# Optimization experiments

Hardware: AMD Instinct MI355X
Metric: run time of the kernel (lower is better)

Reference implementation:

```python
import jax, jax.numpy as jnp
import numpy as np

B, D, K, A = 32768, 256, 1024, 32
MIN_LOG_STD, MAX_LOG_STD = -20.0, 2.0


def setup_inputs() -> dict:
    key = jax.random.key(0)
    ks = jax.random.split(key, 9)
    return {
        "obs": jax.random.normal(ks[0], (B, D), dtype=jnp.float32),
        "mean_C": jax.random.normal(ks[1], (K, D), dtype=jnp.float32),
        "mean_sigma": jnp.abs(jax.random.normal(ks[2], (K,), dtype=jnp.float32)) + 0.1,
        "mean_w": jax.random.normal(ks[3], (A, K), dtype=jnp.float32),
        "mean_b": jax.random.normal(ks[4], (A,), dtype=jnp.float32),
        "std_C": jax.random.normal(ks[5], (K, D), dtype=jnp.float32),
        "std_sigma": jnp.abs(jax.random.normal(ks[6], (K,), dtype=jnp.float32)) + 0.1,
        "std_w": jax.random.normal(ks[7], (A, K), dtype=jnp.float32),
        "std_b": jax.random.normal(ks[8], (A,), dtype=jnp.float32),
    }


def _rbf(x, C, sigma_sq, w, b):
    # r[b,k] = sum_d (x[b,d] - C[k,d])^2, expanded to avoid a [B,K,D] intermediate
    x2 = jnp.sum(x * x, axis=-1, keepdims=True)           # [B,1]
    c2 = jnp.sum(C * C, axis=-1)[None, :]                  # [1,K]
    r = x2 - 2.0 * (x @ C.T) + c2                          # [B,K]
    phi = jnp.exp(-r / (2.0 * jnp.abs(sigma_sq)[None, :]))  # [B,K]
    return phi @ w.T + b[None, :]                          # [B,A]


def reference(obs, mean_C, mean_sigma, mean_w, mean_b,
              std_C, std_sigma, std_w, std_b):
    action_mean = _rbf(obs, mean_C, mean_sigma, mean_w, mean_b)
    std_raw = _rbf(obs, std_C, std_sigma, std_w, std_b)
    action_std = jnp.exp(jnp.clip(std_raw, MIN_LOG_STD, MAX_LOG_STD))
    return jnp.concatenate((action_mean, action_std), axis=-1)  # [B, 2A]
```

## Files before the change

kernel.cpp:

```cpp
#include <hip/hip_runtime.h>


typedef float floatx4 __attribute__((ext_vector_type(4)));
typedef long longx2 __attribute__((ext_vector_type(2)));
typedef unsigned int u32;
typedef unsigned char u8;

constexpr float LOG2E = 1.4426950408889634f;

__device__ __forceinline__ u32 pk_fp8(float a, float b, float c, float d) {
  u32 v = __builtin_amdgcn_cvt_pk_fp8_f32(a, b, 0u, 0);
  v = __builtin_amdgcn_cvt_pk_fp8_f32(c, d, v, 1);
  return v;
}
__device__ __forceinline__ long mk64(u32 lo, u32 hi) {
  return (long)lo | ((long)hi << 32);
}

__global__ void prep(const float* __restrict__ mC, const float* __restrict__ mS,
                     const float* __restrict__ sC, const float* __restrict__ sS,
                     const float* __restrict__ mw, const float* __restrict__ sw,
                     u8* __restrict__ Cb2, float* __restrict__ a2g,
                     float* __restrict__ g2n, u8* __restrict__ wb)
{
  const int blk = blockIdx.x;
  if (blk < 512) {
    const int wq = threadIdx.x >> 6;
    const int t  = threadIdx.x & 63;
    const int b  = blk * 4 + wq;
    const int half = b >> 10;
    const int k = b & 1023;
    const float* src = (half ? sC : mC) + (size_t)k * 256;
    float4 f = *(const float4*)(src + t * 4);
    float ss = f.x*f.x + f.y*f.y + f.z*f.z + f.w*f.w;
    const int ct = b >> 6, row = b & 63;
    const int wvv = row >> 4, cc = row & 15;
    const int ks = t >> 3, qq = (t >> 1) & 3, rr = (t & 1) * 4;
    *(u32*)(Cb2 + (size_t)ct * 16384 + wvv * 4096 + (qq * 16 + cc) * 64 + ks * 8 + rr) =
        pk_fp8(f.x, f.y, f.z, f.w);
    for (int off = 32; off > 0; off >>= 1) ss += __shfl_down(ss, off, 64);
    if (t == 0) {
      float sig = fabsf((half ? sS : mS)[k]);
      float s2 = LOG2E * 0.5f / sig;
      a2g[b] = 2.f * s2;
      g2n[b] = -s2 * ss;
    }
  } else {
    int i0 = (blk - 512) * 1024 + threadIdx.x * 4;
    int half = i0 >> 15;
    int rem  = i0 & 32767;
    const float* src = half ? sw : mw;
    float4 f = *(const float4*)(src + rem);
    ((u32*)wb)[i0 >> 2] = pk_fp8(f.x, f.y, f.z, f.w);
  }
}

__global__ __launch_bounds__(256, 2)
void policy_main(const float* __restrict__ obs,
                 const u8* __restrict__ Cb2,
                 const float* __restrict__ a2g,
                 const float* __restrict__ g2n,
                 const u8* __restrict__ wb,
                 const float* __restrict__ mbias,
                 const float* __restrict__ sbias,
                 float* __restrict__ out)
{
  __shared__ __align__(16) char smem[69888];
  float* x2p = (float*)(smem + 16384);
  float* red = (float*)smem;

  const int tid  = threadIdx.x;
  const int lane = tid & 63;
  const int wv   = tid >> 6;
  const int c    = lane & 15;
  const int q    = lane >> 4;
  const int row0 = blockIdx.x * 64;
  const int kslc = 16 * wv + 4 * q;
  const int cfo  = tid * 64;

  long cfPA[8], cfPB[8], cfQA[8], cfQB[8];
  #pragma unroll
  for (int i = 0; i < 4; ++i) {
    longx2 t0 = *(const longx2*)(Cb2 + cfo + i * 16);
    cfPA[2 * i] = t0.x; cfPA[2 * i + 1] = t0.y;
    longx2 t1 = *(const longx2*)(Cb2 + 16384 + cfo + i * 16);
    cfPB[2 * i] = t1.x; cfPB[2 * i + 1] = t1.y;
  }

  #pragma unroll
  for (int i = 0; i < 4; ++i) {
    int s = i * 256 + tid;
    int row = s >> 4;
    int s16 = s & 15;
    int l16 = s16 ^ (row & 15);
    const float* src = obs + (size_t)(row0 + row) * 256 + l16 * 16;
    float4 f0 = ((const float4*)src)[0];
    float4 f1 = ((const float4*)src)[1];
    float4 f2 = ((const float4*)src)[2];
    float4 f3 = ((const float4*)src)[3];
    uint4 pk;
    pk.x = pk_fp8(f0.x, f0.y, f0.z, f0.w);
    pk.y = pk_fp8(f1.x, f1.y, f1.z, f1.w);
    pk.z = pk_fp8(f2.x, f2.y, f2.z, f2.w);
    pk.w = pk_fp8(f3.x, f3.y, f3.z, f3.w);
    *(uint4*)(smem + s * 16) = pk;
    float p = f0.x*f0.x + f0.y*f0.y + f0.z*f0.z + f0.w*f0.w
            + f1.x*f1.x + f1.y*f1.y + f1.z*f1.z + f1.w*f1.w
            + f2.x*f2.x + f2.y*f2.y + f2.z*f2.z + f2.w*f2.w
            + f3.x*f3.x + f3.y*f3.y + f3.z*f3.z + f3.w*f3.w;
    x2p[row * 16 + s16] = p;
  }
  __syncthreads();

  long ob[4][8];
  #pragma unroll
  for (int nt = 0; nt < 4; ++nt) {
    const int row = nt * 16 + c;
    #pragma unroll
    for (int ks = 0; ks < 8; ++ks) {
      int cc8 = 4 * ks + q;
      int s16 = (cc8 >> 1) ^ (row & 15);
      ob[nt][ks] = *(const long*)(smem + row * 256 + s16 * 16 + (q & 1) * 8);
    }
  }
  if (tid < 64) {
    float s = 0.f;
    #pragma unroll
    for (int j = 0; j < 16; j += 4) {
      float4 a = *(const float4*)(x2p + tid * 16 + j);
      s += a.x + a.y + a.z + a.w;
    }
    x2p[1024 + tid] = s;
  }
  __syncthreads();

  float hx2[4];
  #pragma unroll
  for (int nt = 0; nt < 4; ++nt) hx2[nt] = 0.5f * x2p[1024 + nt * 16 + c];

  const floatx4 Z4 = {0.f, 0.f, 0.f, 0.f};
  floatx4 acc2m[2][4], acc2s[2][4];
  #pragma unroll
  for (int a2i = 0; a2i < 2; ++a2i)
    #pragma unroll
    for (int nt = 0; nt < 4; ++nt) {
      acc2m[a2i][nt] = Z4;
      acc2s[a2i][nt] = Z4;
    }

  u32 pE[4], pc[4];

#define PAIR_BODY(pr, CA, CB, NA, NB, ACC, HB)                                          \
  {                                                                                     \
    const int cte = 2 * (pr);                                                           \
    if ((pr) < 15) {                                                                    \
      const u8* g0 = Cb2 + (size_t)(cte + 2) * 16384 + cfo;                             \
      _Pragma("unroll")                                                                 \
      for (int i = 0; i < 4; ++i) {                                                     \
        longx2 t0 = *(const longx2*)(g0 + i * 16);                                      \
        NA[2 * i] = t0.x; NA[2 * i + 1] = t0.y;                                         \
        longx2 t1 = *(const longx2*)(g0 + 16384 + i * 16);                              \
        NB[2 * i] = t1.x; NB[2 * i + 1] = t1.y;                                         \
      }                                                                                 \
    }                                                                                   \
    float4 a2e = *(const float4*)(a2g + cte * 64 + kslc);                               \
    float4 g2e = *(const float4*)(g2n + cte * 64 + kslc);                               \
    float4 a2o = *(const float4*)(a2g + cte * 64 + 64 + kslc);                          \
    float4 g2o = *(const float4*)(g2n + cte * 64 + 64 + kslc);                          \
    const int kbE = (cte & 15) * 64 + kslc;                                             \
    const u8* wr0 = wb + (size_t)((HB) + c) * 1024 + kbE;                               \
    const u8* wr1 = wb + (size_t)((HB) + 16 + c) * 1024 + kbE;                          \
    u32 w0lo = *(const u32*)wr0, w0hi = *(const u32*)(wr0 + 64);                        \
    u32 w1lo = *(const u32*)wr1, w1hi = *(const u32*)(wr1 + 64);                        \
    floatx4 a1[4];                                                                      \
    a1[0] = __builtin_amdgcn_mfma_f32_16x16x32_fp8_fp8(CA[0], ob[0][0], Z4, 0, 0, 0);   \
    a1[1] = __builtin_amdgcn_mfma_f32_16x16x32_fp8_fp8(CA[0], ob[1][0], Z4, 0, 0, 0);   \
    a1[2] = __builtin_amdgcn_mfma_f32_16x16x32_fp8_fp8(CA[0], ob[2][0], Z4, 0, 0, 0);   \
    a1[3] = __builtin_amdgcn_mfma_f32_16x16x32_fp8_fp8(CA[0], ob[3][0], Z4, 0, 0, 0);   \
    _Pragma("unroll")                                                                   \
    for (int ks = 1; ks < 8; ++ks) {                                                    \
      a1[0] = __builtin_amdgcn_mfma_f32_16x16x32_fp8_fp8(CA[ks], ob[0][ks], a1[0], 0, 0, 0); \
      a1[1] = __builtin_amdgcn_mfma_f32_16x16x32_fp8_fp8(CA[ks], ob[1][ks], a1[1], 0, 0, 0); \
      a1[2] = __builtin_amdgcn_mfma_f32_16x16x32_fp8_fp8(CA[ks], ob[2][ks], a1[2], 0, 0, 0); \
      a1[3] = __builtin_amdgcn_mfma_f32_16x16x32_fp8_fp8(CA[ks], ob[3][ks], a1[3], 0, 0, 0); \
    }                                                                                   \
    _Pragma("unroll")                                                                   \
    for (int nt = 0; nt < 4; ++nt) {                                                    \
      float t0 = a1[nt][0] - hx2[nt], t1 = a1[nt][1] - hx2[nt];                         \
      float t2 = a1[nt][2] - hx2[nt], t3 = a1[nt][3] - hx2[nt];                         \
      pE[nt] = pk_fp8(__builtin_amdgcn_exp2f(fmaf(a2e.x, t0, g2e.x)),                   \
                      __builtin_amdgcn_exp2f(fmaf(a2e.y, t1, g2e.y)),                   \
                      __builtin_amdgcn_exp2f(fmaf(a2e.z, t2, g2e.z)),                   \
                      __builtin_amdgcn_exp2f(fmaf(a2e.w, t3, g2e.w)));                  \
    }                                                                                   \
    a1[0] = __builtin_amdgcn_mfma_f32_16x16x32_fp8_fp8(CB[0], ob[0][0], Z4, 0, 0, 0);   \
    a1[1] = __builtin_amdgcn_mfma_f32_16x16x32_fp8_fp8(CB[0], ob[1][0], Z4, 0, 0, 0);   \
    a1[2] = __builtin_amdgcn_mfma_f32_16x16x32_fp8_fp8(CB[0], ob[2][0], Z4, 0, 0, 0);   \
    a1[3] = __builtin_amdgcn_mfma_f32_16x16x32_fp8_fp8(CB[0], ob[3][0], Z4, 0, 0, 0);   \
    _Pragma("unroll")                                                                   \
    for (int ks = 1; ks < 8; ++ks) {                                                    \
      a1[0] = __builtin_amdgcn_mfma_f32_16x16x32_fp8_fp8(CB[ks], ob[0][ks], a1[0], 0, 0, 0); \
      a1[1] = __builtin_amdgcn_mfma_f32_16x16x32_fp8_fp8(CB[ks], ob[1][ks], a1[1], 0, 0, 0); \
      a1[2] = __builtin_amdgcn_mfma_f32_16x16x32_fp8_fp8(CB[ks], ob[2][ks], a1[2], 0, 0, 0); \
      a1[3] = __builtin_amdgcn_mfma_f32_16x16x32_fp8_fp8(CB[ks], ob[3][ks], a1[3], 0, 0, 0); \
    }                                                                                   \
    _Pragma("unroll")                                                                   \
    for (int nt = 0; nt < 4; ++nt) {                                                    \
      float t0 = a1[nt][0] - hx2[nt], t1 = a1[nt][1] - hx2[nt];                         \
      float t2 = a1[nt][2] - hx2[nt], t3 = a1[nt][3] - hx2[nt];                         \
      pc[nt] = pk_fp8(__builtin_amdgcn_exp2f(fmaf(a2o.x, t0, g2o.x)),                   \
                      __builtin_amdgcn_exp2f(fmaf(a2o.y, t1, g2o.y)),                   \
                      __builtin_amdgcn_exp2f(fmaf(a2o.z, t2, g2o.z)),                   \
                      __builtin_amdgcn_exp2f(fmaf(a2o.w, t3, g2o.w)));                  \
    }                                                                                   \
    { long wA0 = mk64(w0lo, w0hi), wA1 = mk64(w1lo, w1hi);                              \
      _Pragma("unroll")                                                                 \
      for (int nt = 0; nt < 4; ++nt) {                                                  \
        long pb = mk64(pE[nt], pc[nt]);                                                 \
        ACC[0][nt] = __builtin_amdgcn_mfma_f32_16x16x32_fp8_fp8(wA0, pb, ACC[0][nt], 0, 0, 0); \
        ACC[1][nt] = __builtin_amdgcn_mfma_f32_16x16x32_fp8_fp8(wA1, pb, ACC[1][nt], 0, 0, 0); \
      } }                                                                               \
  }

  for (int pr = 0; pr < 8; pr += 2) {
    PAIR_BODY(pr,     cfPA, cfPB, cfQA, cfQB, acc2m, 0)
    PAIR_BODY(pr + 1, cfQA, cfQB, cfPA, cfPB, acc2m, 0)
  }
  for (int pr = 8; pr < 16; pr += 2) {
    PAIR_BODY(pr,     cfPA, cfPB, cfQA, cfQB, acc2s, 32)
    PAIR_BODY(pr + 1, cfQA, cfQB, cfPA, cfPB, acc2s, 32)
  }
#undef PAIR_BODY

  {
    float* myr = red + wv * 4352;
    #pragma unroll
    for (int a2i = 0; a2i < 2; ++a2i)
      #pragma unroll
      for (int nt = 0; nt < 4; ++nt) {
        *(floatx4*)(myr + (nt * 16 + c) * 68 + a2i * 16 + 4 * q)      = acc2m[a2i][nt];
        *(floatx4*)(myr + (nt * 16 + c) * 68 + 32 + a2i * 16 + 4 * q) = acc2s[a2i][nt];
      }
  }
  __syncthreads();

  #pragma unroll
  for (int i = 0; i < 16; ++i) {
    int idx = tid + 256 * i;
    int a = idx & 63;
    int b = idx >> 6;
    float v = red[b * 68 + a] + red[4352 + b * 68 + a] +
              red[8704 + b * 68 + a] + red[13056 + b * 68 + a];
    if (a < 32) {
      v += mbias[a];
    } else {
      v += sbias[a - 32];
      v = fminf(fmaxf(v, -20.f), 2.f);
      v = __builtin_amdgcn_exp2f(v * LOG2E);
    }
    out[(size_t)(row0 + b) * 64 + a] = v;
  }
}

extern "C" void kernel_launch(void* const* d_in, const int* in_sizes, int n_in,
                              void* d_out, int out_size, void* d_ws, size_t ws_size,
                              hipStream_t stream) {
  const float* obs = (const float*)d_in[0];
  const float* mC  = (const float*)d_in[1];
  const float* mS  = (const float*)d_in[2];
  const float* mW  = (const float*)d_in[3];
  const float* mB  = (const float*)d_in[4];
  const float* sC  = (const float*)d_in[5];
  const float* sS  = (const float*)d_in[6];
  const float* sW  = (const float*)d_in[7];
  const float* sB  = (const float*)d_in[8];
  float* out = (float*)d_out;

  u8*    Cb2 = (u8*)d_ws;
  float* a2g = (float*)((char*)d_ws + 2048 * 256);
  float* g2n = a2g + 2048;
  u8*    wb  = (u8*)(g2n + 2048);

  prep<<<576, 256, 0, stream>>>(mC, mS, sC, sS, mW, sW, Cb2, a2g, g2n, wb);
  policy_main<<<512, 256, 0, stream>>>(obs, Cb2, a2g, g2n, wb, mB, sB, out);
}
```

Measured before the change: 130.1 us.

## Switch first distance GEMM from fp8 to int8 MFMA with fixed-scale quantization

Quantizes obs and centers to int8 with a fixed scale (clamped at about ±5) and uses 16x16x64 i8 MFMA instead of 16x16x32 fp8 for the x·C product. This halves the MFMA instruction count for the first GEMM and loads operands as 16-byte vectors. The squared norms and exponent scale factors are recomputed in the quantized domain so the RBF stays consistent. Fixed-scale int8 changes rounding behaviour and clips values beyond the range, which may affect accuracy.

```diff
diff --git a/kernel.cpp b/kernel.cpp
--- a/kernel.cpp
+++ b/kernel.cpp
@@ -2,11 +2,13 @@
 
 
 typedef float floatx4 __attribute__((ext_vector_type(4)));
-typedef long longx2 __attribute__((ext_vector_type(2)));
+typedef int   intx4  __attribute__((ext_vector_type(4)));
 typedef unsigned int u32;
 typedef unsigned char u8;
 
 constexpr float LOG2E = 1.4426950408889634f;
+constexpr float QS    = 25.4f;
+constexpr float SINV2 = (5.0f / 127.0f) * (5.0f / 127.0f);
 
 __device__ __forceinline__ u32 pk_fp8(float a, float b, float c, float d) {
   u32 v = __builtin_amdgcn_cvt_pk_fp8_f32(a, b, 0u, 0);
@@ -15,6 +17,12 @@
 }
 __device__ __forceinline__ long mk64(u32 lo, u32 hi) {
   return (long)lo | ((long)hi << 32);
+}
+__device__ __forceinline__ int q8(float x) {
+  return (int)rintf(fminf(fmaxf(x * QS, -127.f), 127.f));
+}
+__device__ __forceinline__ u32 pk_i8(int a, int b, int c, int d) {
+  return (u32)(a & 255) | ((u32)(b & 255) << 8) | ((u32)(c & 255) << 16) | ((u32)(d & 255) << 24);
 }
 
 __global__ void prep(const float* __restrict__ mC, const float* __restrict__ mS,
@@ -32,18 +40,19 @@
     const int k = b & 1023;
     const float* src = (half ? sC : mC) + (size_t)k * 256;
     float4 f = *(const float4*)(src + t * 4);
-    float ss = f.x*f.x + f.y*f.y + f.z*f.z + f.w*f.w;
+    int i0 = q8(f.x), i1 = q8(f.y), i2 = q8(f.z), i3 = q8(f.w);
     const int ct = b >> 6, row = b & 63;
     const int wvv = row >> 4, cc = row & 15;
-    const int ks = t >> 3, qq = (t >> 1) & 3, rr = (t & 1) * 4;
-    *(u32*)(Cb2 + (size_t)ct * 16384 + wvv * 4096 + (qq * 16 + cc) * 64 + ks * 8 + rr) =
-        pk_fp8(f.x, f.y, f.z, f.w);
-    for (int off = 32; off > 0; off >>= 1) ss += __shfl_down(ss, off, 64);
+    const int ks = t >> 4, qq = (t >> 2) & 3, j0 = (t & 3) * 4;
+    *(u32*)(Cb2 + (size_t)ct * 16384 + wvv * 4096 + (16 * qq + cc) * 64 + 16 * ks + j0) =
+        pk_i8(i0, i1, i2, i3);
+    int is = i0 * i0 + i1 * i1 + i2 * i2 + i3 * i3;
+    for (int off = 32; off > 0; off >>= 1) is += __shfl_down(is, off, 64);
     if (t == 0) {
       float sig = fabsf((half ? sS : mS)[k]);
-      float s2 = LOG2E * 0.5f / sig;
-      a2g[b] = 2.f * s2;
-      g2n[b] = -s2 * ss;
+      float t2 = SINV2 * LOG2E * 0.5f / sig;
+      a2g[b] = 2.f * t2;
+      g2n[b] = -t2 * (float)is;
     }
   } else {
     int i0 = (blk - 512) * 1024 + threadIdx.x * 4;
@@ -78,13 +87,11 @@
   const int kslc = 16 * wv + 4 * q;
   const int cfo  = tid * 64;
 
-  long cfPA[8], cfPB[8], cfQA[8], cfQB[8];
+  intx4 cfPA[4], cfPB[4], cfQA[4], cfQB[4];
   #pragma unroll
   for (int i = 0; i < 4; ++i) {
-    longx2 t0 = *(const longx2*)(Cb2 + cfo + i * 16);
-    cfPA[2 * i] = t0.x; cfPA[2 * i + 1] = t0.y;
-    longx2 t1 = *(const longx2*)(Cb2 + 16384 + cfo + i * 16);
-    cfPB[2 * i] = t1.x; cfPB[2 * i + 1] = t1.y;
+    cfPA[i] = *(const intx4*)(Cb2 + cfo + i * 16);
+    cfPB[i] = *(const intx4*)(Cb2 + 16384 + cfo + i * 16);
   }
 
   #pragma unroll
@@ -98,29 +105,32 @@
     float4 f1 = ((const float4*)src)[1];
     float4 f2 = ((const float4*)src)[2];
     float4 f3 = ((const float4*)src)[3];
+    int a0 = q8(f0.x), a1v = q8(f0.y), a2v = q8(f0.z), a3 = q8(f0.w);
+    int b0 = q8(f1.x), b1 = q8(f1.y), b2 = q8(f1.z), b3 = q8(f1.w);
+    int c0 = q8(f2.x), c1 = q8(f2.y), c2 = q8(f2.z), c3 = q8(f2.w);
+    int d0 = q8(f3.x), d1 = q8(f3.y), d2 = q8(f3.z), d3 = q8(f3.w);
     uint4 pk;
-    pk.x = pk_fp8(f0.x, f0.y, f0.z, f0.w);
-    pk.y = pk_fp8(f1.x, f1.y, f1.z, f1.w);
-    pk.z = pk_fp8(f2.x, f2.y, f2.z, f2.w);
-    pk.w = pk_fp8(f3.x, f3.y, f3.z, f3.w);
+    pk.x = pk_i8(a0, a1v, a2v, a3);
+    pk.y = pk_i8(b0, b1, b2, b3);
+    pk.z = pk_i8(c0, c1, c2, c3);
+    pk.w = pk_i8(d0, d1, d2, d3);
     *(uint4*)(smem + s * 16) = pk;
-    float p = f0.x*f0.x + f0.y*f0.y + f0.z*f0.z + f0.w*f0.w
-            + f1.x*f1.x + f1.y*f1.y + f1.z*f1.z + f1.w*f1.w
-            + f2.x*f2.x + f2.y*f2.y + f2.z*f2.z + f2.w*f2.w
-            + f3.x*f3.x + f3.y*f3.y + f3.z*f3.z + f3.w*f3.w;
-    x2p[row * 16 + s16] = p;
+    int is = a0*a0 + a1v*a1v + a2v*a2v + a3*a3
+           + b0*b0 + b1*b1 + b2*b2 + b3*b3
+           + c0*c0 + c1*c1 + c2*c2 + c3*c3
+           + d0*d0 + d1*d1 + d2*d2 + d3*d3;
+    x2p[row * 16 + s16] = (float)is;
   }
   __syncthreads();
 
-  long ob[4][8];
+  intx4 ob[4][4];
   #pragma unroll
   for (int nt = 0; nt < 4; ++nt) {
     const int row = nt * 16 + c;
     #pragma unroll
-    for (int ks = 0; ks < 8; ++ks) {
-      int cc8 = 4 * ks + q;
-      int s16 = (cc8 >> 1) ^ (row & 15);
-      ob[nt][ks] = *(const long*)(smem + row * 256 + s16 * 16 + (q & 1) * 8);
+    for (int ks = 0; ks < 4; ++ks) {
+      int slot = (4 * ks + q) ^ (row & 15);
+      ob[nt][ks] = *(const intx4*)(smem + row * 256 + slot * 16);
     }
   }
   if (tid < 64) {
@@ -138,6 +148,7 @@
   #pragma unroll
   for (int nt = 0; nt < 4; ++nt) hx2[nt] = 0.5f * x2p[1024 + nt * 16 + c];
 
+  const intx4 Z4i = {0, 0, 0, 0};
   const floatx4 Z4 = {0.f, 0.f, 0.f, 0.f};
   floatx4 acc2m[2][4], acc2s[2][4];
   #pragma unroll
@@ -157,10 +168,8 @@
       const u8* g0 = Cb2 + (size_t)(cte + 2) * 16384 + cfo;                             \
       _Pragma("unroll")                                                                 \
       for (int i = 0; i < 4; ++i) {                                                     \
-        longx2 t0 = *(const longx2*)(g0 + i * 16);                                      \
-        NA[2 * i] = t0.x; NA[2 * i + 1] = t0.y;                                         \
-        longx2 t1 = *(const longx2*)(g0 + 16384 + i * 16);                              \
-        NB[2 * i] = t1.x; NB[2 * i + 1] = t1.y;                                         \
+        NA[i] = *(const intx4*)(g0 + i * 16);                                           \
+        NB[i] = *(const intx4*)(g0 + 16384 + i * 16);                                   \
       }                                                                                 \
     }                                                                                   \
     float4 a2e = *(const float4*)(a2g + cte * 64 + kslc);                               \
@@ -172,42 +181,42 @@
     const u8* wr1 = wb + (size_t)((HB) + 16 + c) * 1024 + kbE;                          \
     u32 w0lo = *(const u32*)wr0, w0hi = *(const u32*)(wr0 + 64);                        \
     u32 w1lo = *(const u32*)wr1, w1hi = *(const u32*)(wr1 + 64);                        \
-    floatx4 a1[4];                                                                      \
-    a1[0] = __builtin_amdgcn_mfma_f32_16x16x32_fp8_fp8(CA[0], ob[0][0], Z4, 0, 0, 0);   \
-    a1[1] = __builtin_amdgcn_mfma_f32_16x16x32_fp8_fp8(CA[0], ob[1][0], Z4, 0, 0, 0);   \
-    a1[2] = __builtin_amdgcn_mfma_f32_16x16x32_fp8_fp8(CA[0], ob[2][0], Z4, 0, 0, 0);   \
-    a1[3] = __builtin_amdgcn_mfma_f32_16x16x32_fp8_fp8(CA[0], ob[3][0], Z4, 0, 0, 0);   \
-    _Pragma("unroll")                                                                   \
-    for (int ks = 1; ks < 8; ++ks) {                                                    \
-      a1[0] = __builtin_amdgcn_mfma_f32_16x16x32_fp8_fp8(CA[ks], ob[0][ks], a1[0], 0, 0, 0); \
-      a1[1] = __builtin_amdgcn_mfma_f32_16x16x32_fp8_fp8(CA[ks], ob[1][ks], a1[1], 0, 0, 0); \
-      a1[2] = __builtin_amdgcn_mfma_f32_16x16x32_fp8_fp8(CA[ks], ob[2][ks], a1[2], 0, 0, 0); \
-      a1[3] = __builtin_amdgcn_mfma_f32_16x16x32_fp8_fp8(CA[ks], ob[3][ks], a1[3], 0, 0, 0); \
+    intx4 a1[4];                                                                        \
+    a1[0] = __builtin_amdgcn_mfma_i32_16x16x64_i8(CA[0], ob[0][0], Z4i, 0, 0, 0);       \
+    a1[1] = __builtin_amdgcn_mfma_i32_16x16x64_i8(CA[0], ob[1][0], Z4i, 0, 0, 0);       \
+    a1[2] = __builtin_amdgcn_mfma_i32_16x16x64_i8(CA[0], ob[2][0], Z4i, 0, 0, 0);       \
+    a1[3] = __builtin_amdgcn_mfma_i32_16x16x64_i8(CA[0], ob[3][0], Z4i, 0, 0, 0);       \
+    _Pragma("unroll")                                                                   \
+    for (int ks = 1; ks < 4; ++ks) {                                                    \
+      a1[0] = __builtin_amdgcn_mfma_i32_16x16x64_i8(CA[ks], ob[0][ks], a1[0], 0, 0, 0); \
+      a1[1] = __builtin_amdgcn_mfma_i32_16x16x64_i8(CA[ks], ob[1][ks], a1[1], 0, 0, 0); \
+      a1[2] = __builtin_amdgcn_mfma_i32_16x16x64_i8(CA[ks], ob[2][ks], a1[2], 0, 0, 0); \
+      a1[3] = __builtin_amdgcn_mfma_i32_16x16x64_i8(CA[ks], ob[3][ks], a1[3], 0, 0, 0); \
     }                                                                                   \
     _Pragma("unroll")                                                                   \
     for (int nt = 0; nt < 4; ++nt) {                                                    \
-      float t0 = a1[nt][0] - hx2[nt], t1 = a1[nt][1] - hx2[nt];                         \
-      float t2 = a1[nt][2] - hx2[nt], t3 = a1[nt][3] - hx2[nt];                         \
+      float t0 = (float)a1[nt][0] - hx2[nt], t1 = (float)a1[nt][1] - hx2[nt];           \
+      float t2 = (float)a1[nt][2] - hx2[nt], t3 = (float)a1[nt][3] - hx2[nt];           \
       pE[nt] = pk_fp8(__builtin_amdgcn_exp2f(fmaf(a2e.x, t0, g2e.x)),                   \
                       __builtin_amdgcn_exp2f(fmaf(a2e.y, t1, g2e.y)),                   \
                       __builtin_amdgcn_exp2f(fmaf(a2e.z, t2, g2e.z)),                   \
                       __builtin_amdgcn_exp2f(fmaf(a2e.w, t3, g2e.w)));                  \
     }                                                                                   \
-    a1[0] = __builtin_amdgcn_mfma_f32_16x16x32_fp8_fp8(CB[0], ob[0][0], Z4, 0, 0, 0);   \
-    a1[1] = __builtin_amdgcn_mfma_f32_16x16x32_fp8_fp8(CB[0], ob[1][0], Z4, 0, 0, 0);   \
-    a1[2] = __builtin_amdgcn_mfma_f32_16x16x32_fp8_fp8(CB[0], ob[2][0], Z4, 0, 0, 0);   \
-    a1[3] = __builtin_amdgcn_mfma_f32_16x16x32_fp8_fp8(CB[0], ob[3][0], Z4, 0, 0, 0);   \
-    _Pragma("unroll")                                                                   \
-    for (int ks = 1; ks < 8; ++ks) {                                                    \
-      a1[0] = __builtin_amdgcn_mfma_f32_16x16x32_fp8_fp8(CB[ks], ob[0][ks], a1[0], 0, 0, 0); \
-      a1[1] = __builtin_amdgcn_mfma_f32_16x16x32_fp8_fp8(CB[ks], ob[1][ks], a1[1], 0, 0, 0); \
-      a1[2] = __builtin_amdgcn_mfma_f32_16x16x32_fp8_fp8(CB[ks], ob[2][ks], a1[2], 0, 0, 0); \
-      a1[3] = __builtin_amdgcn_mfma_f32_16x16x32_fp8_fp8(CB[ks], ob[3][ks], a1[3], 0, 0, 0); \
+    a1[0] = __builtin_amdgcn_mfma_i32_16x16x64_i8(CB[0], ob[0][0], Z4i, 0, 0, 0);       \
+    a1[1] = __builtin_amdgcn_mfma_i32_16x16x64_i8(CB[0], ob[1][0], Z4i, 0, 0, 0);       \
+    a1[2] = __builtin_amdgcn_mfma_i32_16x16x64_i8(CB[0], ob[2][0], Z4i, 0, 0, 0);       \
+    a1[3] = __builtin_amdgcn_mfma_i32_16x16x64_i8(CB[0], ob[3][0], Z4i, 0, 0, 0);       \
+    _Pragma("unroll")                                                                   \
+    for (int ks = 1; ks < 4; ++ks) {                                                    \
+      a1[0] = __builtin_amdgcn_mfma_i32_16x16x64_i8(CB[ks], ob[0][ks], a1[0], 0, 0, 0); \
+      a1[1] = __builtin_amdgcn_mfma_i32_16x16x64_i8(CB[ks], ob[1][ks], a1[1], 0, 0, 0); \
+      a1[2] = __builtin_amdgcn_mfma_i32_16x16x64_i8(CB[ks], ob[2][ks], a1[2], 0, 0, 0); \
+      a1[3] = __builtin_amdgcn_mfma_i32_16x16x64_i8(CB[ks], ob[3][ks], a1[3], 0, 0, 0); \
     }                                                                                   \
     _Pragma("unroll")                                                                   \
     for (int nt = 0; nt < 4; ++nt) {                                                    \
-      float t0 = a1[nt][0] - hx2[nt], t1 = a1[nt][1] - hx2[nt];                         \
-      float t2 = a1[nt][2] - hx2[nt], t3 = a1[nt][3] - hx2[nt];                         \
+      float t0 = (float)a1[nt][0] - hx2[nt], t1 = (float)a1[nt][1] - hx2[nt];           \
+      float t2 = (float)a1[nt][2] - hx2[nt], t3 = (float)a1[nt][3] - hx2[nt];           \
       pc[nt] = pk_fp8(__builtin_amdgcn_exp2f(fmaf(a2o.x, t0, g2o.x)),                   \
                       __builtin_amdgcn_exp2f(fmaf(a2o.y, t1, g2o.y)),                   \
                       __builtin_amdgcn_exp2f(fmaf(a2o.z, t2, g2o.z)),                   \
```

After: 128.2 us. About the same (-1.5%).
